# Optimization experiments

Hardware: AMD Instinct MI355X
Metric: run time of the kernel (lower is better)

Reference implementation:

```python
import jax, jax.numpy as jnp
import numpy as np

D_MODEL = 256; N_HEADS = 8; HEAD_DIM = 32; N_LEVELS = 4; N_POINTS = 4; N_LAYERS = 3; D_FFN = 1024
SHAPES = np.array([[76, 76], [38, 38], [19, 19], [10, 10]], dtype=np.int64)
S_TOTAL = int((SHAPES[:, 0] * SHAPES[:, 1]).sum())  # 7681


def setup_inputs():
    key = jax.random.key(0)
    ks = jax.random.split(key, 12)
    B = 1; C = D_MODEL; M = N_HEADS; Lv = N_LEVELS; P = N_POINTS; L = N_LAYERS; s = 0.02
    starts = np.concatenate([[0], np.cumsum(SHAPES[:, 0] * SHAPES[:, 1])[:-1]]).astype(np.int64)
    inp = {
        "src": jax.random.normal(ks[0], (B, S_TOTAL, C), jnp.float32),
        "pos": jax.random.normal(ks[1], (B, S_TOTAL, C), jnp.float32),
        "valid_ratios": jnp.ones((B, Lv, 2), jnp.float32),
        "spatial_shapes": jnp.asarray(SHAPES),
        "level_start_index": jnp.asarray(starts),
        "padding_mask": jnp.zeros((B, S_TOTAL), bool),
        "W_off": jax.random.normal(ks[2], (L, C, M * Lv * P * 2), jnp.float32) * s,
        "b_off": jax.random.normal(ks[3], (L, M * Lv * P * 2), jnp.float32) * s,
        "W_attn": jax.random.normal(ks[4], (L, C, M * Lv * P), jnp.float32) * s,
        "b_attn": jax.random.normal(ks[5], (L, M * Lv * P), jnp.float32) * s,
        "W_val": jax.random.normal(ks[6], (L, C, C), jnp.float32) * s,
        "b_val": jnp.zeros((L, C), jnp.float32),
        "W_out": jax.random.normal(ks[7], (L, C, C), jnp.float32) * s,
        "b_out": jnp.zeros((L, C), jnp.float32),
        "ln1_g": jnp.ones((L, C), jnp.float32),
        "ln1_b": jnp.zeros((L, C), jnp.float32),
        "W_ff1": jax.random.normal(ks[8], (L, C, D_FFN), jnp.float32) * s,
        "b_ff1": jnp.zeros((L, D_FFN), jnp.float32),
        "W_ff2": jax.random.normal(ks[9], (L, D_FFN, C), jnp.float32) * s,
        "b_ff2": jnp.zeros((L, C), jnp.float32),
        "ln2_g": jnp.ones((L, C), jnp.float32),
        "ln2_b": jnp.zeros((L, C), jnp.float32),
    }
    return inp


def _ln(x, g, b):
    mu = x.mean(-1, keepdims=True)
    var = ((x - mu) ** 2).mean(-1, keepdims=True)
    return (x - mu) * jax.lax.rsqrt(var + 1e-5) * g + b


def _gather(v, idx):
    # v: [B, HW, M, D], idx: [B, S, M, P] -> [B, S, M, P, D], head-specific gather
    B, S, M, P = idx.shape
    def one(vb, ib):
        i2 = ib.transpose(0, 2, 1).reshape(S * P, M, 1)
        o = jnp.take_along_axis(vb, i2, axis=0)  # [S*P, M, D]
        return o.reshape(S, P, M, -1).transpose(0, 2, 1, 3)
    return jax.vmap(one)(v, idx)


def _msda(query, src, mask, ref, shapes, starts, Wo, bo, Wa, ba, Wv, bv, Wout, bout):
    # Multi-scale deformable attention (Deformable-DETR), grid_sample align_corners=False + zero padding
    B, S, C = src.shape
    M, Lv, P, D = N_HEADS, N_LEVELS, N_POINTS, HEAD_DIM
    value = src @ Wv + bv
    value = jnp.where(mask[..., None], 0.0, value).reshape(B, S, M, D)
    off = (query @ Wo + bo).reshape(B, S, M, Lv, P, 2)
    aw = jax.nn.softmax((query @ Wa + ba).reshape(B, S, M, Lv * P), -1).reshape(B, S, M, Lv, P)
    norm = jnp.asarray(shapes[:, ::-1].copy(), jnp.float32)  # (W, H) per level
    loc = ref[:, :, None, :, None, :] + off / norm[None, None, None, :, None, :]  # [B,S,M,Lv,P,2]
    out = jnp.zeros((B, S, M, D), query.dtype)
    for lvl in range(Lv):
        H = int(shapes[lvl, 0]); W = int(shapes[lvl, 1]); st = int(starts[lvl])
        v = value[:, st:st + H * W]  # [B, H*W, M, D]
        l = loc[:, :, :, lvl]  # [B, S, M, P, 2]
        x = l[..., 0] * W - 0.5
        y = l[..., 1] * H - 0.5
        x0 = jnp.floor(x); y0 = jnp.floor(y)
        dx = x - x0; dy = y - y0
        samp = jnp.zeros((B, S, M, P, D), query.dtype)
        for yy, xx, w in ((y0, x0, (1 - dy) * (1 - dx)), (y0, x0 + 1, (1 - dy) * dx),
                          (y0 + 1, x0, dy * (1 - dx)), (y0 + 1, x0 + 1, dy * dx)):
            valid = (xx >= 0) & (xx < W) & (yy >= 0) & (yy < H)
            xi = jnp.clip(xx, 0, W - 1).astype(jnp.int32)
            yi = jnp.clip(yy, 0, H - 1).astype(jnp.int32)
            g = _gather(v, yi * W + xi)
            samp = samp + (w * valid)[..., None] * g
        out = out + (aw[:, :, :, lvl, :, None] * samp).sum(3)
    return out.reshape(B, S, C) @ Wout + bout


def _ref_points(vr, shapes):
    refs = []
    for lvl in range(shapes.shape[0]):
        H = int(shapes[lvl, 0]); W = int(shapes[lvl, 1])
        ry, rx = np.meshgrid(np.linspace(0.5, H - 0.5, H, dtype=np.float32),
                             np.linspace(0.5, W - 0.5, W, dtype=np.float32), indexing="ij")
        rxj = jnp.asarray(rx.reshape(-1))[None] / (vr[:, None, lvl, 0] * W)
        ryj = jnp.asarray(ry.reshape(-1))[None] / (vr[:, None, lvl, 1] * H)
        refs.append(jnp.stack([rxj, ryj], -1))
    ref = jnp.concatenate(refs, 1)  # [B, S, 2]
    return ref[:, :, None] * vr[:, None]  # [B, S, Lv, 2]


def _encoder(src, pos, valid_ratios, shapes, starts, mask, params):
    (W_off, b_off, W_attn, b_attn, W_val, b_val, W_out, b_out,
     ln1_g, ln1_b, W_ff1, b_ff1, W_ff2, b_ff2, ln2_g, ln2_b) = params
    ref = _ref_points(valid_ratios, shapes)
    out = src
    for l in range(N_LAYERS):
        q = out + pos  # with_pos_embed
        a = _msda(q, out, mask, ref, shapes, starts, W_off[l], b_off[l], W_attn[l], b_attn[l],
                  W_val[l], b_val[l], W_out[l], b_out[l])
        out = _ln(out + a, ln1_g[l], ln1_b[l])
        f = jax.nn.relu(out @ W_ff1[l] + b_ff1[l]) @ W_ff2[l] + b_ff2[l]
        out = _ln(out + f, ln2_g[l], ln2_b[l])
    return out


def reference(src, pos, valid_ratios, spatial_shapes, level_start_index, padding_mask,
              W_off, b_off, W_attn, b_attn, W_val, b_val, W_out, b_out,
              ln1_g, ln1_b, W_ff1, b_ff1, W_ff2, b_ff2, ln2_g, ln2_b):
    shapes = np.asarray(spatial_shapes)
    starts = np.asarray(level_start_index)
    params = (W_off, b_off, W_attn, b_attn, W_val, b_val, W_out, b_out,
              ln1_g, ln1_b, W_ff1, b_ff1, W_ff2, b_ff2, ln2_g, ln2_b)
    return _encoder(src, pos, valid_ratios, shapes, starts, padding_mask, params)
```

## Files before the change

### kernel.cpp

```cpp
#include <hip/hip_runtime.h>
#include <hip/hip_bf16.h>
#include <math.h>

#define S_TOTAL 7681

typedef __attribute__((ext_vector_type(8))) short bf16x8;
typedef __attribute__((ext_vector_type(4))) float f32x4;

__device__ __forceinline__ short f2b(float x) {
    union { float f; unsigned u; } v; v.f = x;
    unsigned r = v.u + 0x7FFFu + ((v.u >> 16) & 1u);
    return (short)(r >> 16);
}
__device__ __forceinline__ float b2f(unsigned short u) {
    union { unsigned u; float f; } t; t.u = ((unsigned)u) << 16; return t.f;
}

__device__ __forceinline__ void gll16(const short* g, short* l) {
    __builtin_amdgcn_global_load_lds(
        (const __attribute__((address_space(1))) unsigned int*)g,
        (__attribute__((address_space(3))) unsigned int*)l,
        16, 0, 0);
}

#define SBAR() asm volatile("s_barrier" ::: "memory")

#define MFMA16(a, b, c) __builtin_amdgcn_mfma_f32_16x16x32_bf16(a, b, c, 0, 0, 0)

__global__ __launch_bounds__(256) void transpose_cvt_kernel(
    const float* __restrict__ s0, const float* __restrict__ s1,
    const float* __restrict__ s2, const float* __restrict__ s3,
    const float* __restrict__ s4, const float* __restrict__ s5,
    short* __restrict__ d0, short* __restrict__ d1, short* __restrict__ d2,
    short* __restrict__ d3, short* __restrict__ d4, short* __restrict__ d5,
    const float4* __restrict__ csrc, const float4* __restrict__ cpos,
    float4* __restrict__ co, ushort4* __restrict__ cxb, ushort4* __restrict__ cqb)
{
    const int z = blockIdx.z;
    int t = blockIdx.x;
    if (t >= 736) {
        const int n4 = S_TOTAL * 64;
        int i = (z * 641 + (t - 736)) * 256 + threadIdx.x;
        if (i < n4) {
            float4 v = csrc[i], p = cpos[i];
            co[i] = v;
            ushort4 h, hq;
            h.x = (unsigned short)f2b(v.x); h.y = (unsigned short)f2b(v.y);
            h.z = (unsigned short)f2b(v.z); h.w = (unsigned short)f2b(v.w);
            hq.x = (unsigned short)f2b(v.x + p.x); hq.y = (unsigned short)f2b(v.y + p.y);
            hq.z = (unsigned short)f2b(v.z + p.z); hq.w = (unsigned short)f2b(v.w + p.w);
            cxb[i] = h;
            cqb[i] = hq;
        }
        return;
    }
    const float* src; short* dst; int K, N, lt;
    if (t < 64)       { src = s0 + (size_t)z * 65536;  dst = d0 + (size_t)z * 65536;  K = 256;  N = 256;  lt = t; }
    else if (t < 128) { src = s1 + (size_t)z * 65536;  dst = d1 + (size_t)z * 98304;  K = 256;  N = 256;  lt = t - 64; }
    else if (t < 160) { src = s2 + (size_t)z * 32768;  dst = d2 + (size_t)z * 98304;  K = 256;  N = 128;  lt = t - 128; }
    else if (t < 224) { src = s3 + (size_t)z * 65536;  dst = d3 + (size_t)z * 65536;  K = 256;  N = 256;  lt = t - 160; }
    else if (t < 480) { src = s4 + (size_t)z * 262144; dst = d4 + (size_t)z * 262144; K = 256;  N = 1024; lt = t - 224; }
    else              { src = s5 + (size_t)z * 262144; dst = d5 + (size_t)z * 262144; K = 1024; N = 256;  lt = t - 480; }
    const int ntx = N >> 5;
    const int tk = (lt / ntx) << 5, tn = (lt % ntx) << 5;
    __shared__ float tile[32][33];
    const int cx = threadIdx.x & 31, cy = threadIdx.x >> 5;
    #pragma unroll
    for (int i = 0; i < 32; i += 8)
        tile[cy + i][cx] = src[(size_t)(tk + cy + i) * N + tn + cx];
    __syncthreads();
    #pragma unroll
    for (int i = 0; i < 32; i += 8)
        dst[(size_t)(tn + cy + i) * K + tk + cx] = f2b(tile[cx][cy + i]);
}

__global__ __launch_bounds__(256) void gemm_va_kernel(
    const short* __restrict__ xb, const short* __restrict__ qb,
    const short* __restrict__ Wt_val, const short* __restrict__ Wt_oa,
    const float* __restrict__ b_val, const float* __restrict__ b_off,
    const float* __restrict__ b_attn,
    short* __restrict__ value_bf, float* __restrict__ offbuf, int M)
{
    const int grp = (blockIdx.y >= 4);
    const short* A  = grp ? qb : xb;
    const short* Wt = grp ? Wt_oa : Wt_val;
    const int colBase = (grp ? (blockIdx.y - 4) : blockIdx.y) * 64;
    const int K = 256;

    __shared__ __align__(16) short As[2][128 * 64];
    __shared__ __align__(16) short Bs[2][64 * 64];

    const int tid = threadIdx.x;
    const int lane = tid & 63;
    const int wave = tid >> 6;
    const int rowBase = blockIdx.x * 128;

    const int sr = lane >> 3;
    const int sc = ((lane & 7) ^ sr) << 3;

    const short* gA[4];
    #pragma unroll
    for (int c = 0; c < 4; ++c)
        gA[c] = A + (size_t)min(rowBase + wave * 32 + c * 8 + sr, M - 1) * K + sc;
    const short* gB[2];
    #pragma unroll
    for (int c = 0; c < 2; ++c)
        gB[c] = Wt + (size_t)(colBase + wave * 16 + c * 8 + sr) * K + sc;

    const int frow = lane & 15;
    const int g4 = lane >> 4;
    const int r7 = frow & 7;
    const int wm = wave * 32;

    f32x4 acc[2][4] = {};

    auto stage = [&](int buf, int k0) {
        #pragma unroll
        for (int c = 0; c < 4; ++c)
            gll16(gA[c] + k0, &As[buf][(wave * 32 + c * 8) * 64]);
        #pragma unroll
        for (int c = 0; c < 2; ++c)
            gll16(gB[c] + k0, &Bs[buf][(wave * 16 + c * 8) * 64]);
    };

    stage(0, 0);

    int cur = 0;
    for (int k0 = 0; k0 < K; k0 += 64) {
        if (k0 + 64 < K) {
            stage(cur ^ 1, k0 + 64);
            asm volatile("s_waitcnt vmcnt(6)" ::: "memory");
        } else {
            asm volatile("s_waitcnt vmcnt(0)" ::: "memory");
        }
        SBAR();
        #pragma unroll
        for (int kk8 = 0; kk8 < 8; kk8 += 4) {
            const int ua = (((kk8 + g4) ^ r7) << 3);
            bf16x8 af0 = *(const bf16x8*)&As[cur][(wm + frow) * 64 + ua];
            bf16x8 af1 = *(const bf16x8*)&As[cur][(wm + 16 + frow) * 64 + ua];
            #pragma unroll
            for (int j = 0; j < 4; ++j) {
                bf16x8 bfj = *(const bf16x8*)&Bs[cur][(j * 16 + frow) * 64 + ua];
                acc[0][j] = MFMA16(af0, bfj, acc[0][j]);
                acc[1][j] = MFMA16(af1, bfj, acc[1][j]);
            }
        }
        SBAR();
        cur ^= 1;
    }

    const int erow = (lane >> 4) * 4;
    const int ecol = lane & 15;
    #pragma unroll
    for (int mi = 0; mi < 2; ++mi) {
        #pragma unroll
        for (int j = 0; j < 4; ++j) {
            int col = colBase + j * 16 + ecol;
            float bias = grp ? (col < 256 ? b_off[col] : b_attn[col - 256]) : b_val[col];
            #pragma unroll
            for (int r = 0; r < 4; ++r) {
                int row = rowBase + wm + mi * 16 + erow + r;
                if (row < M) {
                    float v = acc[mi][j][r] + bias;
                    if (grp) offbuf[(size_t)row * 384 + col] = v;
                    else     value_bf[(size_t)row * 256 + col] = f2b(v);
                }
            }
        }
    }
}

template<int RELU, int OUTBF>
__global__ __launch_bounds__(256) void gemm_kernel(
    const short* __restrict__ A, const short* __restrict__ Wt,
    const float* __restrict__ bias, void* __restrict__ Cv,
    int M, int N, int K)
{
    __shared__ __align__(16) short As[2][128 * 64];
    __shared__ __align__(16) short Bs[2][64 * 64];

    const int tid = threadIdx.x;
    const int lane = tid & 63;
    const int wave = tid >> 6;
    const int rowBase = blockIdx.x * 128;
    const int colBase = blockIdx.y * 64;

    const int sr = lane >> 3;
    const int sc = ((lane & 7) ^ sr) << 3;

    const short* gA[4];
    #pragma unroll
    for (int c = 0; c < 4; ++c)
        gA[c] = A + (size_t)min(rowBase + wave * 32 + c * 8 + sr, M - 1) * K + sc;
    const short* gB[2];
    #pragma unroll
    for (int c = 0; c < 2; ++c)
        gB[c] = Wt + (size_t)(colBase + wave * 16 + c * 8 + sr) * K + sc;

    const int frow = lane & 15;
    const int g4 = lane >> 4;
    const int r7 = frow & 7;
    const int wm = wave * 32;

    f32x4 acc[2][4] = {};

    auto stage = [&](int buf, int k0) {
        #pragma unroll
        for (int c = 0; c < 4; ++c)
            gll16(gA[c] + k0, &As[buf][(wave * 32 + c * 8) * 64]);
        #pragma unroll
        for (int c = 0; c < 2; ++c)
            gll16(gB[c] + k0, &Bs[buf][(wave * 16 + c * 8) * 64]);
    };

    stage(0, 0);

    int cur = 0;
    for (int k0 = 0; k0 < K; k0 += 64) {
        if (k0 + 64 < K) {
            stage(cur ^ 1, k0 + 64);
            asm volatile("s_waitcnt vmcnt(6)" ::: "memory");
        } else {
            asm volatile("s_waitcnt vmcnt(0)" ::: "memory");
        }
        SBAR();
        #pragma unroll
        for (int kk8 = 0; kk8 < 8; kk8 += 4) {
            const int ua = (((kk8 + g4) ^ r7) << 3);
            bf16x8 af0 = *(const bf16x8*)&As[cur][(wm + frow) * 64 + ua];
            bf16x8 af1 = *(const bf16x8*)&As[cur][(wm + 16 + frow) * 64 + ua];
            #pragma unroll
            for (int j = 0; j < 4; ++j) {
                bf16x8 bfj = *(const bf16x8*)&Bs[cur][(j * 16 + frow) * 64 + ua];
                acc[0][j] = MFMA16(af0, bfj, acc[0][j]);
                acc[1][j] = MFMA16(af1, bfj, acc[1][j]);
            }
        }
        SBAR();
        cur ^= 1;
    }

    const int erow = (lane >> 4) * 4;
    const int ecol = lane & 15;
    #pragma unroll
    for (int mi = 0; mi < 2; ++mi) {
        #pragma unroll
        for (int j = 0; j < 4; ++j) {
            #pragma unroll
            for (int r = 0; r < 4; ++r) {
                int row = rowBase + wm + mi * 16 + erow + r;
                if (row < M) {
                    int col = colBase + j * 16 + ecol;
                    float v = acc[mi][j][r] + bias[col];
                    if (RELU) v = fmaxf(v, 0.f);
                    if (OUTBF) ((short*)Cv)[(size_t)row * N + col] = f2b(v);
                    else       ((float*)Cv)[(size_t)row * N + col] = v;
                }
            }
        }
    }
}

template<int WRITEQ>
__global__ __launch_bounds__(256) void gemm_ln_kernel(
    const short* __restrict__ A, const short* __restrict__ Wt,
    const float* __restrict__ bias, const float* __restrict__ g,
    const float* __restrict__ bln, const float* __restrict__ pos,
    float* __restrict__ out, short* __restrict__ xb, short* __restrict__ qb,
    int M, int K)
{
    __shared__ __align__(16) short As[2][16 * 64];
    __shared__ __align__(16) short Bs[2][256 * 64];
    __shared__ float rsum[16][4], rsq[16][4], smu[16], srs[16];

    const int tid = threadIdx.x;
    const int lane = tid & 63;
    const int wave = tid >> 6;
    const int rowBase = blockIdx.x * 16;

    const int sr = lane >> 3;
    const int sc = ((lane & 7) ^ sr) << 3;

    const short* gA = A + (size_t)min(rowBase + wave * 8 + sr, M - 1) * K + sc;
    const short* gB[8];
    #pragma unroll
    for (int c = 0; c < 8; ++c)
        gB[c] = Wt + (size_t)(wave * 64 + c * 8 + sr) * K + sc;

    const int frow = lane & 15;
    const int g4 = lane >> 4;
    const int r7 = frow & 7;

    f32x4 acc[4] = {};

    auto stage = [&](int buf, int k0) {
        if (wave < 2) gll16(gA + k0, &As[buf][(wave * 8) * 64]);
        #pragma unroll
        for (int c = 0; c < 8; ++c)
            gll16(gB[c] + k0, &Bs[buf][(wave * 64 + c * 8) * 64]);
    };

    stage(0, 0);

    int cur = 0;
    for (int k0 = 0; k0 < K; k0 += 64) {
        if (k0 + 64 < K) {
            stage(cur ^ 1, k0 + 64);
            if (wave < 2) asm volatile("s_waitcnt vmcnt(9)" ::: "memory");
            else          asm volatile("s_waitcnt vmcnt(8)" ::: "memory");
        } else {
            asm volatile("s_waitcnt vmcnt(0)" ::: "memory");
        }
        SBAR();
        #pragma unroll
        for (int kk8 = 0; kk8 < 8; kk8 += 4) {
            const int ua = (((kk8 + g4) ^ r7) << 3);
            bf16x8 af = *(const bf16x8*)&As[cur][frow * 64 + ua];
            #pragma unroll
            for (int j = 0; j < 4; ++j) {
                bf16x8 bfj = *(const bf16x8*)&Bs[cur][(wave * 64 + j * 16 + frow) * 64 + ua];
                acc[j] = MFMA16(af, bfj, acc[j]);
            }
        }
        SBAR();
        cur ^= 1;
    }

    const int erow = (lane >> 4) * 4;
    const int ecol = lane & 15;
    float x[4][4];
    #pragma unroll
    for (int j = 0; j < 4; ++j)
        #pragma unroll
        for (int r = 0; r < 4; ++r) {
            int row = rowBase + erow + r;
            int col = wave * 64 + j * 16 + ecol;
            float res = (row < M) ? out[(size_t)row * 256 + col] : 0.f;
            x[j][r] = acc[j][r] + bias[col] + res;
        }

    #pragma unroll
    for (int r = 0; r < 4; ++r) {
        float s1 = x[0][r] + x[1][r] + x[2][r] + x[3][r];
        float s2 = x[0][r]*x[0][r] + x[1][r]*x[1][r]
                 + x[2][r]*x[2][r] + x[3][r]*x[3][r];
        #pragma unroll
        for (int o = 1; o < 16; o <<= 1) {
            s1 += __shfl_xor(s1, o);
            s2 += __shfl_xor(s2, o);
        }
        if ((lane & 15) == 0) {
            rsum[erow + r][wave] = s1;
            rsq [erow + r][wave] = s2;
        }
    }
    __syncthreads();
    if (tid < 16) {
        float S1 = rsum[tid][0] + rsum[tid][1] + rsum[tid][2] + rsum[tid][3];
        float S2 = rsq[tid][0] + rsq[tid][1] + rsq[tid][2] + rsq[tid][3];
        float mu = S1 * (1.f / 256.f);
        smu[tid] = mu;
        srs[tid] = rsqrtf(S2 * (1.f / 256.f) - mu * mu + 1e-5f);
    }
    __syncthreads();

    #pragma unroll
    for (int r = 0; r < 4; ++r) {
        int lrow = erow + r;
        int row = rowBase + lrow;
        if (row >= M) continue;
        float mu = smu[lrow], rs = srs[lrow];
        #pragma unroll
        for (int j = 0; j < 4; ++j) {
            int col = wave * 64 + j * 16 + ecol;
            float y = (x[j][r] - mu) * rs * g[col] + bln[col];
            out[(size_t)row * 256 + col] = y;
            xb[(size_t)row * 256 + col] = f2b(y);
            if (WRITEQ)
                qb[(size_t)row * 256 + col] = f2b(y + pos[(size_t)row * 256 + col]);
        }
    }
}

__global__ __launch_bounds__(256) void msda_kernel(
    const short* __restrict__ value, const float* __restrict__ offb,
    short* __restrict__ msdab)
{
    __shared__ float soff[8 * 384];

    const int bid = blockIdx.x;
    const int sb = (bid & 7) * 121 + (bid >> 3);
    const int q0 = sb * 8;
    if (q0 >= S_TOTAL) return;
    const int tid = threadIdx.x;

    {
        const float4* src4 = (const float4*)offb;
        #pragma unroll
        for (int i = tid; i < 768; i += 256) {
            int qi = i / 96, j = i - qi * 96;
            int q = min(q0 + qi, S_TOTAL - 1);
            *(float4*)&soff[qi * 384 + j * 4] = src4[(size_t)q * 96 + j];
        }
    }
    __syncthreads();

    if (tid < 64) {
        const int qi = tid >> 3, m = tid & 7;
        float* lg = &soff[qi * 384 + 256 + m * 16];
        float mx = -1e30f;
        #pragma unroll
        for (int k = 0; k < 16; ++k) mx = fmaxf(mx, lg[k]);
        float e[16], sum = 0.f;
        #pragma unroll
        for (int k = 0; k < 16; ++k) { e[k] = expf(lg[k] - mx); sum += e[k]; }
        float inv = 1.f / sum;
        #pragma unroll
        for (int k = 0; k < 16; ++k) lg[k] = e[k] * inv;
    }
    __syncthreads();

    const int lane = tid & 63;
    const int qi = (tid >> 6) * 2 + (lane >> 5);
    const int q = q0 + qi;
    if (q >= S_TOTAL) return;
    const int l32 = lane & 31;
    const int h = l32 >> 2, dg = l32 & 3;
    const short* vcol = value + h * 32 + dg * 8;

    float refx, refy;
    if (q < 5776)      { int t = q;        int r = t / 76, c = t % 76; refx = (c + 0.5f) / 76.f; refy = (r + 0.5f) / 76.f; }
    else if (q < 7220) { int t = q - 5776; int r = t / 38, c = t % 38; refx = (c + 0.5f) / 38.f; refy = (r + 0.5f) / 38.f; }
    else if (q < 7581) { int t = q - 7220; int r = t / 19, c = t % 19; refx = (c + 0.5f) / 19.f; refy = (r + 0.5f) / 19.f; }
    else               { int t = q - 7581; int r = t / 10, c = t % 10; refx = (c + 0.5f) / 10.f; refy = (r + 0.5f) / 10.f; }

    const float* so = &soff[qi * 384];
    float a[8] = {};
    #pragma unroll
    for (int pt = 0; pt < 16; ++pt) {
        const int LVL_HW[4] = {76, 38, 19, 10};
        const int LVL_ST[4] = {0, 5776, 7220, 7581};
        const int lvl = pt >> 2;
        const int W = LVL_HW[lvl];
        const int base = LVL_ST[lvl];
        const float fW = (float)W;
        const int i = h * 16 + pt;

        float ox = so[i * 2];
        float oy = so[i * 2 + 1];
        float aw = so[256 + i];

        float x = refx * fW + ox - 0.5f;
        float y = refy * fW + oy - 0.5f;
        float x0f = floorf(x), y0f = floorf(y);
        int x0 = (int)x0f, y0 = (int)y0f;
        float dx = x - x0f, dy = y - y0f;

        bool vx0 = (x0 >= 0) & (x0 < W);
        bool vx1 = (x0 >= -1) & (x0 < W - 1);
        bool vy0 = (y0 >= 0) & (y0 < W);
        bool vy1 = (y0 >= -1) & (y0 < W - 1);
        int xc0 = min(max(x0, 0), W - 1), xc1 = min(max(x0 + 1, 0), W - 1);
        int yc0 = min(max(y0, 0), W - 1), yc1 = min(max(y0 + 1, 0), W - 1);
        int i00 = base + yc0 * W + xc0;
        int i01 = base + yc0 * W + xc1;
        int i10 = base + yc1 * W + xc0;
        int i11 = base + yc1 * W + xc1;
        float w00 = (vy0 && vx0) ? (1.f - dy) * (1.f - dx) * aw : 0.f;
        float w01 = (vy0 && vx1) ? (1.f - dy) * dx * aw : 0.f;
        float w10 = (vy1 && vx0) ? dy * (1.f - dx) * aw : 0.f;
        float w11 = (vy1 && vx1) ? dy * dx * aw : 0.f;

        bf16x8 v0 = *(const bf16x8*)(vcol + ((size_t)i00 << 8));
        bf16x8 v1 = *(const bf16x8*)(vcol + ((size_t)i01 << 8));
        bf16x8 v2 = *(const bf16x8*)(vcol + ((size_t)i10 << 8));
        bf16x8 v3 = *(const bf16x8*)(vcol + ((size_t)i11 << 8));
        #pragma unroll
        for (int e = 0; e < 8; ++e)
            a[e] += w00 * b2f((unsigned short)v0[e]) + w01 * b2f((unsigned short)v1[e])
                  + w10 * b2f((unsigned short)v2[e]) + w11 * b2f((unsigned short)v3[e]);
    }
    bf16x8 o;
    #pragma unroll
    for (int e = 0; e < 8; ++e) o[e] = f2b(a[e]);
    *(bf16x8*)(msdab + (size_t)q * 256 + h * 32 + dg * 8) = o;
}

extern "C" void kernel_launch(void* const* d_in, const int* in_sizes, int n_in,
                              void* d_out, int out_size, void* d_ws, size_t ws_size,
                              hipStream_t stream) {
    const float* src    = (const float*)d_in[0];
    const float* pos    = (const float*)d_in[1];
    const float* W_off  = (const float*)d_in[6];
    const float* b_off  = (const float*)d_in[7];
    const float* W_attn = (const float*)d_in[8];
    const float* b_attn = (const float*)d_in[9];
    const float* W_val  = (const float*)d_in[10];
    const float* b_val  = (const float*)d_in[11];
    const float* W_out  = (const float*)d_in[12];
    const float* b_out  = (const float*)d_in[13];
    const float* ln1_g  = (const float*)d_in[14];
    const float* ln1_b  = (const float*)d_in[15];
    const float* W_ff1  = (const float*)d_in[16];
    const float* b_ff1  = (const float*)d_in[17];
    const float* W_ff2  = (const float*)d_in[18];
    const float* b_ff2  = (const float*)d_in[19];
    const float* ln2_g  = (const float*)d_in[20];
    const float* ln2_b  = (const float*)d_in[21];

    const size_t S = S_TOTAL;
    float* out = (float*)d_out;

    short* wt = (short*)d_ws;
    short* Wt_val = wt;
    short* Wt_oa  = wt + 196608;
    short* Wt_out = wt + 491520;
    short* Wt_ff1 = wt + 688128;
    short* Wt_ff2 = wt + 1474560;
    float* fbase  = (float*)d_ws + 1131648;
    short* xb       = (short*)fbase;
    short* qb       = (short*)(fbase + 128 * S);
    short* value_bf = (short*)(fbase + 256 * S);
    float* offb     = fbase + 384 * S;
    short* msdab    = (short*)(fbase + 768 * S);
    short* hid      = (short*)(fbase + 256 * S);

    transpose_cvt_kernel<<<dim3(1377, 1, 3), 256, 0, stream>>>(
        W_val, W_off, W_attn, W_out, W_ff1, W_ff2,
        Wt_val, Wt_oa, Wt_oa + 65536, Wt_out, Wt_ff1, Wt_ff2,
        (const float4*)src, (const float4*)pos,
        (float4*)out, (ushort4*)xb, (ushort4*)qb);

    const int MB = (S_TOTAL + 127) / 128;
    const int LB = (S_TOTAL + 15) / 16;

    for (int l = 0; l < 3; ++l) {
        gemm_va_kernel<<<dim3(MB, 10), 256, 0, stream>>>(
            xb, qb, Wt_val + (size_t)l * 65536, Wt_oa + (size_t)l * 98304,
            b_val + (size_t)l * 256, b_off + (size_t)l * 256, b_attn + (size_t)l * 128,
            value_bf, offb, S_TOTAL);
        msda_kernel<<<968, 256, 0, stream>>>(value_bf, offb, msdab);
        gemm_ln_kernel<0><<<LB, 256, 0, stream>>>(
            msdab, Wt_out + (size_t)l * 65536, b_out + (size_t)l * 256,
            ln1_g + (size_t)l * 256, ln1_b + (size_t)l * 256, pos,
            out, xb, qb, S_TOTAL, 256);
        gemm_kernel<1, 1><<<dim3(MB, 16), 256, 0, stream>>>(
            xb, Wt_ff1 + (size_t)l * 262144, b_ff1 + (size_t)l * 1024, hid,
            S_TOTAL, 1024, 256);
        gemm_ln_kernel<1><<<LB, 256, 0, stream>>>(
            hid, Wt_ff2 + (size_t)l * 262144, b_ff2 + (size_t)l * 256,
            ln2_g + (size_t)l * 256, ln2_b + (size_t)l * 256, pos,
            out, xb, qb, S_TOTAL, 1024);
    }
}
```

Before: 388.3 us.

## Restructure MSDA kernel to one query per wave with padded LDS and shuffle softmax

The deformable-attention sampling kernel now assigns one query per wavefront, with each lane handling 4 channels instead of 8, which doubles the thread count and the grid size. Offsets and logits are staged per wave into padded shared memory to avoid bank conflicts. The per-head softmax runs across 8 lanes using shuffles rather than serially in 64 threads, and the block-wide __syncthreads barriers are removed. The cost is narrower 8-byte gathers per sample, so more load instructions are issued for the same data.

After: 367.7 us (median of 2 runs). -5.3%, faster.

```diff
diff --git a/kernel.cpp b/kernel.cpp
--- a/kernel.cpp
+++ b/kernel.cpp
@@ -387,47 +387,57 @@
     const short* __restrict__ value, const float* __restrict__ offb,
     short* __restrict__ msdab)
 {
-    __shared__ float soff[8 * 384];
+    __shared__ float soff[4 * 400];
 
     const int bid = blockIdx.x;
-    const int sb = (bid & 7) * 121 + (bid >> 3);
-    const int q0 = sb * 8;
-    if (q0 >= S_TOTAL) return;
+    const int sb = (bid < 1920) ? ((bid & 7) * 240 + (bid >> 3)) : bid;
+    const int q0 = sb * 4;
     const int tid = threadIdx.x;
+    const int lane = tid & 63;
+    const int wave = tid >> 6;
+
+    const int q = q0 + wave;
+    const int qc = min(q, S_TOTAL - 1);
+    float* row = &soff[wave * 400];
 
     {
-        const float4* src4 = (const float4*)offb;
-        #pragma unroll
-        for (int i = tid; i < 768; i += 256) {
-            int qi = i / 96, j = i - qi * 96;
-            int q = min(q0 + qi, S_TOTAL - 1);
-            *(float4*)&soff[qi * 384 + j * 4] = src4[(size_t)q * 96 + j];
-        }
-    }
-    __syncthreads();
-
-    if (tid < 64) {
-        const int qi = tid >> 3, m = tid & 7;
-        float* lg = &soff[qi * 384 + 256 + m * 16];
-        float mx = -1e30f;
-        #pragma unroll
-        for (int k = 0; k < 16; ++k) mx = fmaxf(mx, lg[k]);
-        float e[16], sum = 0.f;
-        #pragma unroll
-        for (int k = 0; k < 16; ++k) { e[k] = expf(lg[k] - mx); sum += e[k]; }
+        const float4* src4 = (const float4*)offb + (size_t)qc * 96;
+        #pragma unroll
+        for (int i = lane; i < 96; i += 64) {
+            float4 v = src4[i];
+            int s = i * 4;
+            float vv[4] = {v.x, v.y, v.z, v.w};
+            #pragma unroll
+            for (int k = 0; k < 4; ++k) {
+                int sk = s + k;
+                int dst;
+                if (sk < 256) { int m = sk >> 5, r = sk & 31; dst = m * 33 + r; }
+                else          { int j = sk - 256; int m = j >> 4, r = j & 15; dst = 264 + m * 17 + r; }
+                row[dst] = vv[k];
+            }
+        }
+    }
+
+    {
+        const int m = lane >> 3, j = lane & 7;
+        float* lg = row + 264 + m * 17;
+        float e0 = lg[j], e1 = lg[j + 8];
+        float mx = fmaxf(e0, e1);
+        #pragma unroll
+        for (int o = 1; o < 8; o <<= 1) mx = fmaxf(mx, __shfl_xor(mx, o));
+        e0 = expf(e0 - mx); e1 = expf(e1 - mx);
+        float sum = e0 + e1;
+        #pragma unroll
+        for (int o = 1; o < 8; o <<= 1) sum += __shfl_xor(sum, o);
         float inv = 1.f / sum;
-        #pragma unroll
-        for (int k = 0; k < 16; ++k) lg[k] = e[k] * inv;
-    }
-    __syncthreads();
-
-    const int lane = tid & 63;
-    const int qi = (tid >> 6) * 2 + (lane >> 5);
-    const int q = q0 + qi;
+        lg[j] = e0 * inv;
+        lg[j + 8] = e1 * inv;
+    }
+
     if (q >= S_TOTAL) return;
-    const int l32 = lane & 31;
-    const int h = l32 >> 2, dg = l32 & 3;
-    const short* vcol = value + h * 32 + dg * 8;
+
+    const int h = lane >> 3, dg = lane & 7;
+    const short* vcol = value + h * 32 + dg * 4;
 
     float refx, refy;
     if (q < 5776)      { int t = q;        int r = t / 76, c = t % 76; refx = (c + 0.5f) / 76.f; refy = (r + 0.5f) / 76.f; }
@@ -435,8 +445,7 @@
     else if (q < 7581) { int t = q - 7220; int r = t / 19, c = t % 19; refx = (c + 0.5f) / 19.f; refy = (r + 0.5f) / 19.f; }
     else               { int t = q - 7581; int r = t / 10, c = t % 10; refx = (c + 0.5f) / 10.f; refy = (r + 0.5f) / 10.f; }
 
-    const float* so = &soff[qi * 384];
-    float a[8] = {};
+    float a[4] = {};
     #pragma unroll
     for (int pt = 0; pt < 16; ++pt) {
         const int LVL_HW[4] = {76, 38, 19, 10};
@@ -445,11 +454,10 @@
         const int W = LVL_HW[lvl];
         const int base = LVL_ST[lvl];
         const float fW = (float)W;
-        const int i = h * 16 + pt;
-
-        float ox = so[i * 2];
-        float oy = so[i * 2 + 1];
-        float aw = so[256 + i];
+
+        float ox = row[h * 33 + pt * 2];
+        float oy = row[h * 33 + pt * 2 + 1];
+        float aw = row[264 + h * 17 + pt];
 
         float x = refx * fW + ox - 0.5f;
         float y = refy * fW + oy - 0.5f;
@@ -472,19 +480,22 @@
         float w10 = (vy1 && vx0) ? dy * (1.f - dx) * aw : 0.f;
         float w11 = (vy1 && vx1) ? dy * dx * aw : 0.f;
 
-        bf16x8 v0 = *(const bf16x8*)(vcol + ((size_t)i00 << 8));
-        bf16x8 v1 = *(const bf16x8*)(vcol + ((size_t)i01 << 8));
-        bf16x8 v2 = *(const bf16x8*)(vcol + ((size_t)i10 << 8));
-        bf16x8 v3 = *(const bf16x8*)(vcol + ((size_t)i11 << 8));
-        #pragma unroll
-        for (int e = 0; e < 8; ++e)
-            a[e] += w00 * b2f((unsigned short)v0[e]) + w01 * b2f((unsigned short)v1[e])
-                  + w10 * b2f((unsigned short)v2[e]) + w11 * b2f((unsigned short)v3[e]);
-    }
-    bf16x8 o;
-    #pragma unroll
-    for (int e = 0; e < 8; ++e) o[e] = f2b(a[e]);
-    *(bf16x8*)(msdab + (size_t)q * 256 + h * 32 + dg * 8) = o;
+        ushort4 v0 = *(const ushort4*)(vcol + ((size_t)i00 << 8));
+        ushort4 v1 = *(const ushort4*)(vcol + ((size_t)i01 << 8));
+        ushort4 v2 = *(const ushort4*)(vcol + ((size_t)i10 << 8));
+        ushort4 v3 = *(const ushort4*)(vcol + ((size_t)i11 << 8));
+        const unsigned short* p0 = (const unsigned short*)&v0;
+        const unsigned short* p1 = (const unsigned short*)&v1;
+        const unsigned short* p2 = (const unsigned short*)&v2;
+        const unsigned short* p3 = (const unsigned short*)&v3;
+        #pragma unroll
+        for (int e = 0; e < 4; ++e)
+            a[e] += w00 * b2f(p0[e]) + w01 * b2f(p1[e])
+                  + w10 * b2f(p2[e]) + w11 * b2f(p3[e]);
+    }
+    short4 o;
+    o.x = f2b(a[0]); o.y = f2b(a[1]); o.z = f2b(a[2]); o.w = f2b(a[3]);
+    *(short4*)(msdab + (size_t)q * 256 + h * 32 + dg * 4) = o;
 }
 
 extern "C" void kernel_launch(void* const* d_in, const int* in_sizes, int n_in,
@@ -534,13 +545,14 @@
 
     const int MB = (S_TOTAL + 127) / 128;
     const int LB = (S_TOTAL + 15) / 16;
+    const int SB = (S_TOTAL + 3) / 4;
 
     for (int l = 0; l < 3; ++l) {
         gemm_va_kernel<<<dim3(MB, 10), 256, 0, stream>>>(
             xb, qb, Wt_val + (size_t)l * 65536, Wt_oa + (size_t)l * 98304,
             b_val + (size_t)l * 256, b_off + (size_t)l * 256, b_attn + (size_t)l * 128,
             value_bf, offb, S_TOTAL);
-        msda_kernel<<<968, 256, 0, stream>>>(value_bf, offb, msdab);
+        msda_kernel<<<SB, 256, 0, stream>>>(value_bf, offb, msdab);
         gemm_ln_kernel<0><<<LB, 256, 0, stream>>>(
             msdab, Wt_out + (size_t)l * 65536, b_out + (size_t)l * 256,
             ln1_g + (size_t)l * 256, ln1_b + (size_t)l * 256, pos,
```
